# Optimization experiments

Hardware: AMD Instinct MI355X
Metric: run time of the kernel (lower is better)

Reference implementation:

```python
import jax, jax.numpy as jnp
import numpy as np

N = 6144
IN_DIM = 512
CHANNELS = 4
C_DIM = 64
ITERATIONS = 3
BETA = 1.0
EDGE_P = 0.005  # ~30 avg degree


def _l2norm(x):
    # F.normalize(dim=-1): x / max(||x||_2, eps)
    return x / jnp.maximum(jnp.linalg.norm(x, axis=-1, keepdims=True), 1e-12)


def setup_inputs() -> dict:
    key = jax.random.key(0)
    kf, ka, kw, kb = jax.random.split(key, 4)
    features = jax.random.normal(kf, (N, IN_DIM), dtype=jnp.float32)
    # sparse 0/1 adjacency, densified (module calls adj.to_dense())
    adj = (jax.random.uniform(ka, (N, N)) < EDGE_P).astype(jnp.int32)
    # per-channel weights/biases, init ~ N(0, 1) as in init_parameters
    W = jax.random.normal(kw, (CHANNELS, IN_DIM, C_DIM), dtype=jnp.float32)
    b = jax.random.normal(kb, (CHANNELS, 1, C_DIM), dtype=jnp.float32)
    return {"features": features, "adj": adj, "W": W, "b": b}


def reference(features, adj, W, b):
    mask = adj > 0  # [N, N]
    # per-channel projection + row L2-normalize -> [C, N, K]
    feats = _l2norm(jnp.einsum('nd,cdk->cnk', features, W) + b)
    for _ in range(ITERATIONS):
        # per-channel dense self-attention scores, masked by adjacency
        att = jnp.einsum('cnk,cmk->cnm', feats, feats) / BETA  # [C, N, N]
        att = jnp.where(mask[None, :, :], att, 0.0)
        # softmax across channels (torch dim=2 after cat == channel axis)
        att = jax.nn.softmax(att, axis=0)
        att = jnp.where(mask[None, :, :], att, 0.0)
        # aggregate and renormalize
        feats = _l2norm(feats + jnp.einsum('cnm,cmk->cnk', att, feats))
    # concat channels along feature dim -> [N, C*K]
    return jnp.transpose(feats, (1, 0, 2)).reshape(N, CHANNELS * C_DIM)
```

## Files before the change

### kernel.cpp

```cpp
#include <hip/hip_runtime.h>
#include <hip/hip_bf16.h>
#include <math.h>

#define NN      6144
#define IN_DIM  512
#define CH      4
#define CDIM    64
#define NODE    256
#define PR      16
#define PBLK    (NN / PR)
#define MAXD    96

typedef int v4i __attribute__((ext_vector_type(4)));

__device__ __forceinline__ unsigned short f2bf(float x) {
    union { float f; unsigned int u; } v; v.f = x;
    const unsigned int r = v.u + 0x7FFFu + ((v.u >> 16) & 1u);
    return (unsigned short)(r >> 16);
}
__device__ __forceinline__ float bflo(unsigned int u) {
    union { unsigned int u; float f; } v; v.u = u << 16; return v.f;
}
__device__ __forceinline__ float bfhi(unsigned int u) {
    union { unsigned int u; float f; } v; v.u = u & 0xFFFF0000u; return v.f;
}
__device__ __forceinline__ void unpack8(uint4 u, float* o) {
    o[0] = bflo(u.x); o[1] = bfhi(u.x);
    o[2] = bflo(u.y); o[3] = bfhi(u.y);
    o[4] = bflo(u.z); o[5] = bfhi(u.z);
    o[6] = bflo(u.w); o[7] = bfhi(u.w);
}

template <int CTRL>
__device__ __forceinline__ float dppadd(float v) {
    return v + __int_as_float(
        __builtin_amdgcn_update_dpp(0, __float_as_int(v), CTRL, 0xF, 0xF, true));
}

__global__ __launch_bounds__(256) void proj_ell_kernel(
    const float* __restrict__ feat,
    const float* __restrict__ W,
    const float* __restrict__ bias,
    const int*   __restrict__ adj,
    unsigned short* __restrict__ outbf,
    int*   __restrict__ deg,
    int*   __restrict__ cols)
{
    __shared__ float lds[PR * IN_DIM];
    const int t = threadIdx.x;

    if (blockIdx.x < PBLK) {
        const int row0 = blockIdx.x * PR;
        {
            const float4* src = (const float4*)(feat + (size_t)row0 * IN_DIM);
            float4* dst = (float4*)lds;
#pragma unroll
            for (int i = 0; i < (PR * IN_DIM / 4) / 256; ++i)
                dst[t + i * 256] = src[t + i * 256];
        }
        __syncthreads();

        const int g  = t >> 6;
        const int q  = t & 63;
        const int c  = q >> 4;
        const int k0 = (q & 15) * 4;

        float acc[4][4];
#pragma unroll
        for (int r = 0; r < 4; ++r)
#pragma unroll
            for (int j = 0; j < 4; ++j) acc[r][j] = 0.0f;

        const float* Wc   = W + (size_t)c * IN_DIM * CDIM + k0;
        const float* arow = lds + g * 4 * IN_DIM;

        for (int d = 0; d < IN_DIM; d += 4) {
            const float4 w0 = *(const float4*)(Wc + (size_t)(d + 0) * CDIM);
            const float4 w1 = *(const float4*)(Wc + (size_t)(d + 1) * CDIM);
            const float4 w2 = *(const float4*)(Wc + (size_t)(d + 2) * CDIM);
            const float4 w3 = *(const float4*)(Wc + (size_t)(d + 3) * CDIM);
#pragma unroll
            for (int r = 0; r < 4; ++r) {
                const float4 a = *(const float4*)(arow + r * IN_DIM + d);
                acc[r][0] = fmaf(a.x, w0.x, fmaf(a.y, w1.x, fmaf(a.z, w2.x, fmaf(a.w, w3.x, acc[r][0]))));
                acc[r][1] = fmaf(a.x, w0.y, fmaf(a.y, w1.y, fmaf(a.z, w2.y, fmaf(a.w, w3.y, acc[r][1]))));
                acc[r][2] = fmaf(a.x, w0.z, fmaf(a.y, w1.z, fmaf(a.z, w2.z, fmaf(a.w, w3.z, acc[r][2]))));
                acc[r][3] = fmaf(a.x, w0.w, fmaf(a.y, w1.w, fmaf(a.z, w2.w, fmaf(a.w, w3.w, acc[r][3]))));
            }
            if ((d & 15) == 12) __syncthreads();
        }

        const float4 bv = *(const float4*)(bias + c * CDIM + k0);
#pragma unroll
        for (int r = 0; r < 4; ++r) {
            acc[r][0] += bv.x; acc[r][1] += bv.y; acc[r][2] += bv.z; acc[r][3] += bv.w;
            float ss = acc[r][0] * acc[r][0] + acc[r][1] * acc[r][1]
                     + acc[r][2] * acc[r][2] + acc[r][3] * acc[r][3];
            ss += __shfl_xor(ss, 1, 64);
            ss += __shfl_xor(ss, 2, 64);
            ss += __shfl_xor(ss, 4, 64);
            ss += __shfl_xor(ss, 8, 64);
            const float rn = __builtin_amdgcn_rsqf(fmaxf(ss, 1e-24f));
            ushort4 res;
            res.x = f2bf(acc[r][0] * rn); res.y = f2bf(acc[r][1] * rn);
            res.z = f2bf(acc[r][2] * rn); res.w = f2bf(acc[r][3] * rn);
            *(ushort4*)(outbf + (size_t)(row0 + g * 4 + r) * NODE + c * CDIM + k0) = res;
        }
    } else {
        int* cnt = (int*)lds;
        const int n = blockIdx.x - PBLK;
        if (t == 0) *cnt = 0;
        __syncthreads();

        const v4i* row = (const v4i*)(adj + (size_t)n * NN);
        int* rowcols = cols + (size_t)n * MAXD;
        for (int i = t; i < NN / 4; i += 256) {
            const v4i v = __builtin_nontemporal_load(&row[i]);
            if (v.x | v.y | v.z | v.w) {
                const int base = i * 4;
                if (v.x) { int p = atomicAdd(cnt, 1); if (p < MAXD) rowcols[p] = base + 0; }
                if (v.y) { int p = atomicAdd(cnt, 1); if (p < MAXD) rowcols[p] = base + 1; }
                if (v.z) { int p = atomicAdd(cnt, 1); if (p < MAXD) rowcols[p] = base + 2; }
                if (v.w) { int p = atomicAdd(cnt, 1); if (p < MAXD) rowcols[p] = base + 3; }
            }
        }
        __syncthreads();
        if (t == 0) deg[n] = min(*cnt, MAXD);
    }
}

template <bool LAST>
__global__ __launch_bounds__(256) void iter_kernel(
    const unsigned short* __restrict__ fin,
    unsigned short* __restrict__ fout,
    float* __restrict__ fout32,
    const int* __restrict__ deg,
    const int* __restrict__ cols)
{
    const int wv   = threadIdx.x >> 6;
    const int lane = threadIdx.x & 63;
    const int n    = blockIdx.x * 4 + wv;
    const int nb   = lane >> 4;
    const int cj   = lane & 15;

    float qv[16], av[16];
    {
        const uint4* qp = (const uint4*)(fin + (size_t)n * NODE + cj * 16);
        unpack8(qp[0], qv); unpack8(qp[1], qv + 8);
    }
#pragma unroll
    for (int i = 0; i < 16; ++i) av[i] = 0.0f;

    const int d = deg[n];
    const int* cl = cols + (size_t)n * MAXD;
    const int nch = (d + 3) >> 2;

    bool val = nb < d;
    uint4 fa, fb;
    {
        const int m = val ? cl[nb] : 0;
        const uint4* fp = (const uint4*)(fin + (size_t)m * NODE + cj * 16);
        fa = fp[0]; fb = fp[1];
    }

    for (int ch = 0; ch < nch; ++ch) {
        const bool more = (ch + 1 < nch);
        bool valn = false;
        uint4 ga, gb;
        if (more) {
            const int idx = (ch + 1) * 4 + nb;
            valn = idx < d;
            const int m2 = valn ? cl[idx] : 0;
            const uint4* gp = (const uint4*)(fin + (size_t)m2 * NODE + cj * 16);
            ga = gp[0]; gb = gp[1];
        }

        float fv[16];
        unpack8(fa, fv); unpack8(fb, fv + 8);

        float p = 0.0f;
#pragma unroll
        for (int i = 0; i < 16; ++i) p = fmaf(qv[i], fv[i], p);
        p = dppadd<0xB1>(p);
        p = dppadd<0x4E>(p);
        const float e = __expf(p);
        float s = dppadd<0x124>(e);
        s = dppadd<0x128>(s);
        const float w = val ? e * __builtin_amdgcn_rcpf(s) : 0.0f;

#pragma unroll
        for (int i = 0; i < 16; ++i) av[i] = fmaf(w, fv[i], av[i]);

        if (more) { fa = ga; fb = gb; val = valn; }
    }

#pragma unroll
    for (int i = 0; i < 16; ++i) {
        av[i] += __shfl_xor(av[i], 16, 64);
        av[i] += __shfl_xor(av[i], 32, 64);
    }
#pragma unroll
    for (int i = 0; i < 16; ++i) av[i] += qv[i];

    float ss = 0.0f;
#pragma unroll
    for (int i = 0; i < 16; ++i) ss = fmaf(av[i], av[i], ss);
    ss = dppadd<0xB1>(ss);
    ss = dppadd<0x4E>(ss);
    const float rn = __builtin_amdgcn_rsqf(fmaxf(ss, 1e-24f));

    const float4 s0 = make_float4(av[0]  * rn, av[1]  * rn, av[2]  * rn, av[3]  * rn);
    const float4 s1 = make_float4(av[4]  * rn, av[5]  * rn, av[6]  * rn, av[7]  * rn);
    const float4 s2 = make_float4(av[8]  * rn, av[9]  * rn, av[10] * rn, av[11] * rn);
    const float4 s3 = make_float4(av[12] * rn, av[13] * rn, av[14] * rn, av[15] * rn);
    const float4 o = (nb == 0) ? s0 : (nb == 1) ? s1 : (nb == 2) ? s2 : s3;

    if (LAST) {
        *(float4*)(fout32 + (size_t)n * NODE + cj * 16 + nb * 4) = o;
    } else {
        ushort4 ob;
        ob.x = f2bf(o.x); ob.y = f2bf(o.y); ob.z = f2bf(o.z); ob.w = f2bf(o.w);
        *(ushort4*)(fout + (size_t)n * NODE + cj * 16 + nb * 4) = ob;
    }
}

extern "C" void kernel_launch(void* const* d_in, const int* in_sizes, int n_in,
                              void* d_out, int out_size, void* d_ws, size_t ws_size,
                              hipStream_t stream) {
    const float* features = (const float*)d_in[0];
    const int*   adj      = (const int*)d_in[1];
    const float* W        = (const float*)d_in[2];
    const float* b        = (const float*)d_in[3];
    float* out = (float*)d_out;

    unsigned short* featsA = (unsigned short*)d_ws;
    unsigned short* featsB = featsA + (size_t)NN * NODE;
    int* deg  = (int*)(featsB + (size_t)NN * NODE);
    int* cols = deg + NN;

    proj_ell_kernel<<<PBLK + NN, 256, 0, stream>>>(features, W, b, adj,
                                                   featsA, deg, cols);
    iter_kernel<false><<<NN / 4, 256, 0, stream>>>(featsA, featsB, nullptr, deg, cols);
    iter_kernel<false><<<NN / 4, 256, 0, stream>>>(featsB, featsA, nullptr, deg, cols);
    iter_kernel<true ><<<NN / 4, 256, 0, stream>>>(featsA, nullptr, out, deg, cols);
}
```

Measured before the change: 274.8 us.

## Interleave projection and ELL-build blocks and read features directly from global

Projection blocks are interleaved with adjacency-scan blocks at a stride of 17, so the compute-bound projection work is spread across the grid alongside the bandwidth-bound ELL construction instead of all running first. The projection no longer stages its 16 feature rows in a 32 KB LDS buffer; each wave reads its rows from global memory through a wave-uniform base pointer, which removes the staging copy and the LDS footprint and should raise occupancy. The adjacency scan loop is fully unrolled. The trade-off is that feature reads now hit global memory or cache rather than LDS, and correctness depends on the host launching PBLK*17 blocks in total.

```diff
diff --git a/kernel.cpp b/kernel.cpp
--- a/kernel.cpp
+++ b/kernel.cpp
@@ -10,6 +10,7 @@
 #define PR      16
 #define PBLK    (NN / PR)
 #define MAXD    96
+#define GSTRIDE 17
 
 typedef int v4i __attribute__((ext_vector_type(4)));
 
@@ -46,20 +47,13 @@
     int*   __restrict__ deg,
     int*   __restrict__ cols)
 {
-    __shared__ float lds[PR * IN_DIM];
-    const int t = threadIdx.x;
-
-    if (blockIdx.x < PBLK) {
-        const int row0 = blockIdx.x * PR;
-        {
-            const float4* src = (const float4*)(feat + (size_t)row0 * IN_DIM);
-            float4* dst = (float4*)lds;
-#pragma unroll
-            for (int i = 0; i < (PR * IN_DIM / 4) / 256; ++i)
-                dst[t + i * 256] = src[t + i * 256];
-        }
-        __syncthreads();
-
+    __shared__ int cnt;
+    const int t   = threadIdx.x;
+    const int bid = blockIdx.x;
+
+    if (bid % GSTRIDE == 0) {
+        const int gb   = bid / GSTRIDE;
+        const int row0 = gb * PR;
         const int g  = t >> 6;
         const int q  = t & 63;
         const int c  = q >> 4;
@@ -71,8 +65,10 @@
 #pragma unroll
             for (int j = 0; j < 4; ++j) acc[r][j] = 0.0f;
 
-        const float* Wc   = W + (size_t)c * IN_DIM * CDIM + k0;
-        const float* arow = lds + g * 4 * IN_DIM;
+        const float* Wc = W + (size_t)c * IN_DIM * CDIM + k0;
+        int rowbase = (row0 + g * 4) * IN_DIM;
+        rowbase = __builtin_amdgcn_readfirstlane(rowbase);
+        const float* arow = feat + rowbase;
 
         for (int d = 0; d < IN_DIM; d += 4) {
             const float4 w0 = *(const float4*)(Wc + (size_t)(d + 0) * CDIM);
@@ -107,25 +103,26 @@
             *(ushort4*)(outbf + (size_t)(row0 + g * 4 + r) * NODE + c * CDIM + k0) = res;
         }
     } else {
-        int* cnt = (int*)lds;
-        const int n = blockIdx.x - PBLK;
-        if (t == 0) *cnt = 0;
+        const int n = bid - bid / GSTRIDE - 1;
+        if (t == 0) cnt = 0;
         __syncthreads();
 
         const v4i* row = (const v4i*)(adj + (size_t)n * NN);
         int* rowcols = cols + (size_t)n * MAXD;
-        for (int i = t; i < NN / 4; i += 256) {
+#pragma unroll
+        for (int it = 0; it < (NN / 4) / 256; ++it) {
+            const int i = t + it * 256;
             const v4i v = __builtin_nontemporal_load(&row[i]);
             if (v.x | v.y | v.z | v.w) {
                 const int base = i * 4;
-                if (v.x) { int p = atomicAdd(cnt, 1); if (p < MAXD) rowcols[p] = base + 0; }
-                if (v.y) { int p = atomicAdd(cnt, 1); if (p < MAXD) rowcols[p] = base + 1; }
-                if (v.z) { int p = atomicAdd(cnt, 1); if (p < MAXD) rowcols[p] = base + 2; }
-                if (v.w) { int p = atomicAdd(cnt, 1); if (p < MAXD) rowcols[p] = base + 3; }
+                if (v.x) { int p = atomicAdd(&cnt, 1); if (p < MAXD) rowcols[p] = base + 0; }
+                if (v.y) { int p = atomicAdd(&cnt, 1); if (p < MAXD) rowcols[p] = base + 1; }
+                if (v.z) { int p = atomicAdd(&cnt, 1); if (p < MAXD) rowcols[p] = base + 2; }
+                if (v.w) { int p = atomicAdd(&cnt, 1); if (p < MAXD) rowcols[p] = base + 3; }
             }
         }
         __syncthreads();
-        if (t == 0) deg[n] = min(*cnt, MAXD);
+        if (t == 0) deg[n] = min(cnt, MAXD);
     }
 }
 
```

Result: slower. 314.2 us (+14.4%).
